# Kernel optimization log

Measured on AMD Instinct MI355X. Metric: run time of the kernel, lower is better.

Reference implementation:

```python
import jax, jax.numpy as jnp
import numpy as np

# Model dims (match init_kwargs)
B, L, C = 4, 4096, 1024   # batch, seq_len, dim
M = 128                   # memory_dim
P = 4                     # n_persistent
S = 64                    # segment_size
H = 8                     # num_heads in nn.MultiheadAttention


def _ln(x, g, b, eps=1e-5):
    mu = jnp.mean(x, -1, keepdims=True)
    var = jnp.mean((x - mu) ** 2, -1, keepdims=True)
    return (x - mu) * jax.lax.rsqrt(var + eps) * g + b


def setup_inputs() -> dict:
    key = jax.random.key(0)
    ks = jax.random.split(key, 16)
    def n(k, shape, s=0.02):
        return jax.random.normal(k, shape, jnp.float32) * s
    return {
        "x": jax.random.normal(ks[0], (B, L, C), jnp.float32),
        "persistent_memory": n(ks[1], (1, P, C)),
        "Wq": n(ks[2], (C, C)),            # query_proj (no bias)
        "Wk": n(ks[3], (C, C)),            # key_proj (no bias)
        "Wv": n(ks[4], (C, C)),            # value_proj (no bias)
        # NeuralMemoryModule.memory_net: Linear(C->M), SiLU, LN(M), Linear(M->M), LN(M)
        "mem_W1": n(ks[5], (M, C)), "mem_b1": jnp.zeros((M,)),
        "mem_ln1_g": jnp.ones((M,)), "mem_ln1_b": jnp.zeros((M,)),
        "mem_W2": n(ks[6], (M, M)), "mem_b2": jnp.zeros((M,)),
        "mem_ln2_g": jnp.ones((M,)), "mem_ln2_b": jnp.zeros((M,)),
        "mem_out_W": n(ks[7], (C, M)), "mem_out_b": jnp.zeros((C,)),
        "memory_state": jnp.zeros((1, M)),  # persistent buffer (zeros at init)
        # nn.MultiheadAttention in/out projections
        "mha_Wq": n(ks[8], (C, C)), "mha_bq": jnp.zeros((C,)),
        "mha_Wk": n(ks[9], (C, C)), "mha_bk": jnp.zeros((C,)),
        "mha_Wv": n(ks[10], (C, C)), "mha_bv": jnp.zeros((C,)),
        "mha_Wo": n(ks[11], (C, C)), "mha_bo": jnp.zeros((C,)),
        "gn_g": jnp.ones((C,)), "gn_b": jnp.zeros((C,)),   # gate_norm
        "gate_W": n(ks[12], (C, C)), "gate_b": jnp.zeros((C,)),
        "out_W": n(ks[13], (C, C)), "out_b": jnp.zeros((C,)),
    }


def reference(x, persistent_memory, Wq, Wk, Wv,
              mem_W1, mem_b1, mem_ln1_g, mem_ln1_b,
              mem_W2, mem_b2, mem_ln2_g, mem_ln2_b,
              mem_out_W, mem_out_b, memory_state,
              mha_Wq, mha_bq, mha_Wk, mha_bk, mha_Wv, mha_bv, mha_Wo, mha_bo,
              gn_g, gn_b, gate_W, gate_b, out_W, out_b):
    Bx, Lx, Cx = x.shape
    n_seg = Lx // S
    # Eval-mode: memory_state is frozen, so all segments are independent ->
    # process every segment in parallel instead of a Python loop over L.
    xs = x.reshape(Bx * n_seg, S, Cx)           # [N, S, C]
    q_seg = xs @ Wq.T                            # query_proj
    # retrieve from long-term memory: memory_net(queries) + memory_state -> output_proj
    h = jax.nn.silu(q_seg @ mem_W1.T + mem_b1)
    h = _ln(h, mem_ln1_g, mem_ln1_b)
    h = h @ mem_W2.T + mem_b2
    h = _ln(h, mem_ln2_g, mem_ln2_b)             # [N, S, M]
    retrieved = (h + memory_state[0]) @ mem_out_W.T + mem_out_b  # [N, S, C]
    # context = [retrieved_memory, persistent_memory, current_segment]
    pm = jnp.broadcast_to(persistent_memory, (Bx * n_seg, P, Cx))
    context = jnp.concatenate([retrieved, pm, xs], axis=1)       # [N, T, C], T=S+P+S
    k_in = context @ Wk.T
    v_in = context @ Wv.T
    T = context.shape[1]
    hd = Cx // H
    q = (q_seg @ mha_Wq.T + mha_bq).reshape(-1, S, H, hd)
    k = (k_in @ mha_Wk.T + mha_bk).reshape(-1, T, H, hd)
    v = (v_in @ mha_Wv.T + mha_bv).reshape(-1, T, H, hd)
    scores = jnp.einsum('nshd,nthd->nhst', q, k) / jnp.sqrt(jnp.float32(hd))
    attn = jnp.einsum('nhst,nthd->nshd', jax.nn.softmax(scores, -1), v)
    attn = attn.reshape(-1, S, Cx) @ mha_Wo.T + mha_bo           # [N, S, C]
    # learned gate blend + output projection
    gate = jax.nn.sigmoid(_ln(attn, gn_g, gn_b) @ gate_W.T + gate_b)
    out = (gate * attn + xs) @ out_W.T + out_b
    return out.reshape(Bx, Lx, Cx)
```

## Files before the change

### kernel.cpp

```cpp
#include <hip/hip_runtime.h>
#include <hip/hip_bf16.h>
#include <math.h>


using bf16 = __hip_bfloat16;

typedef __attribute__((ext_vector_type(8))) short bf16x8;
typedef __attribute__((ext_vector_type(4))) float f32x4;

__device__ __forceinline__ float ldf(const bf16* p) { return __bfloat162float(*p); }
__device__ __forceinline__ float ldf(const float* p) { return *p; }
__device__ __forceinline__ void stf(bf16* p, float v) { *p = __float2bfloat16(v); }
__device__ __forceinline__ void stf(float* p, float v) { *p = v; }
__device__ __forceinline__ float b2f(const bf16& b) { return __bfloat162float(b); }
__device__ __forceinline__ float bsf(short s) {
  union { unsigned u; float f; } cv;
  cv.u = (unsigned)(unsigned short)s << 16;
  return cv.f;
}

enum { ACT_NONE = 0, ACT_SILU = 1, ACT_SIGMOID = 2, ACT_GATE = 3, ACT_PSILU = 4 };

__global__ void detect_kernel(const unsigned short* g, int* flag) {
  if (threadIdx.x == 0) *flag = (g[0] != 0) ? 1 : 0;
}

struct ConvArgs {
  const void* src[29];
  bf16* dst[29];
  int n[29];
  int bstart[30];
};

__global__ __launch_bounds__(256) void convall_kernel(ConvArgs a, const int* __restrict__ flag) {
  int b = blockIdx.x;
  int ti = 0;
  while (ti < 28 && b >= a.bstart[ti + 1]) ++ti;
  int i = (b - a.bstart[ti]) * 256 + threadIdx.x;
  if (i >= a.n[ti]) return;
  if (*flag) a.dst[ti][i] = ((const bf16*)a.src[ti])[i];
  else a.dst[ti][i] = __float2bfloat16(((const float*)a.src[ti])[i]);
}

__global__ __launch_bounds__(256) void conv_kernel(
    const void* __restrict__ src, bf16* __restrict__ dst, int n, size_t src_off,
    const int* __restrict__ flag) {
  int i = blockIdx.x * 256 + threadIdx.x;
  if (i >= n) return;
  if (*flag) dst[i] = ((const bf16*)src)[src_off + i];
  else dst[i] = __float2bfloat16(((const float*)src)[src_off + i]);
}

__global__ __launch_bounds__(256) void pack_bias4(
    const bf16* __restrict__ bk, const bf16* __restrict__ bv,
    const bf16* __restrict__ bq, const bf16* __restrict__ b1,
    bf16* __restrict__ o) {
  int j = blockIdx.x * 256 + threadIdx.x;
  if (j >= 3200) return;
  float v;
  if (j < 1024) v = b2f(bk[j]);
  else if (j < 2048) v = b2f(bv[j - 1024]);
  else if (j < 3072) v = b2f(bq[j - 2048]);
  else v = b2f(b1[j - 3072]);
  o[j] = __float2bfloat16(v);
}

__global__ __launch_bounds__(256) void transpose_kernel(
    const bf16* __restrict__ srcb, bf16* __restrict__ dstb, int rows, int cols) {
  __shared__ unsigned short t[64][72];
  const unsigned short* src = (const unsigned short*)srcb;
  unsigned short* dst = (unsigned short*)dstb;
  const int r0 = blockIdx.y * 64, c0 = blockIdx.x * 64;
  for (int e = threadIdx.x; e < 64 * 8; e += 256) {
    int r = e >> 3, c8 = e & 7;
    uint4 v = *(const uint4*)(src + (size_t)(r0 + r) * cols + c0 + c8 * 8);
    *(uint4*)&t[r][c8 * 8] = v;
  }
  __syncthreads();
  for (int e = threadIdx.x; e < 64 * 8; e += 256) {
    int c = e >> 3, r8 = (e & 7) * 8;
    unsigned short v[8];
#pragma unroll
    for (int j = 0; j < 8; ++j) v[j] = t[r8 + j][c];
    *(uint4*)(dst + (size_t)(c0 + c) * rows + r0 + r8) = *(uint4*)v;
  }
}

__global__ __launch_bounds__(256) void kpvp_kernel(
    const bf16* __restrict__ pmb, const bf16* __restrict__ mobb,
    const bf16* __restrict__ Wb, const bf16* __restrict__ bias4b,
    bf16* __restrict__ kp, bf16* __restrict__ vp, bf16* __restrict__ bkv)
{
  const short* pm = (const short*)pmb;
  const short* mob = (const short*)mobb;
  const short* W = (const short*)Wb;
  const int wave = threadIdx.x >> 6, lane = threadIdx.x & 63;
  const int c = blockIdx.x * 4 + wave;
  const short* wrow = W + (size_t)c * 1024 + lane * 16;
  const bf16x8 w0 = *(const bf16x8*)wrow;
  const bf16x8 w1 = *(const bf16x8*)(wrow + 8);
  float acc[5];
#pragma unroll
  for (int m = 0; m < 5; ++m) {
    const short* prow = (m < 4) ? (pm + m * 1024 + lane * 16) : (mob + lane * 16);
    const bf16x8 p0 = *(const bf16x8*)prow;
    const bf16x8 p1 = *(const bf16x8*)(prow + 8);
    float s = 0.f;
#pragma unroll
    for (int j = 0; j < 8; ++j) s += bsf(w0[j]) * bsf(p0[j]) + bsf(w1[j]) * bsf(p1[j]);
    acc[m] = s;
  }
#pragma unroll
  for (int d = 1; d < 64; d <<= 1) {
#pragma unroll
    for (int m = 0; m < 5; ++m) acc[m] += __shfl_xor(acc[m], d);
  }
  if (lane == 0) {
    const float bv = b2f(bias4b[c]);
    bf16* dst = (c < 1024) ? (kp + c) : (vp + (c - 1024));
#pragma unroll
    for (int m = 0; m < 4; ++m) stf(dst + m * 1024, acc[m] + bv);
    stf(&bkv[c], acc[4] + bv);
  }
}

__device__ __forceinline__ void gl_lds16(const short* g, short* l) {
  __builtin_amdgcn_global_load_lds(
      (const __attribute__((address_space(1))) void*)g,
      (__attribute__((address_space(3))) void*)l, 16, 0, 0);
}

template <typename TC, int ACT, bool HAS_BIAS>
__global__ __launch_bounds__(256) void mgemm(
    const bf16* __restrict__ Ab, const bf16* __restrict__ Bw,
    const bf16* __restrict__ bias, TC* __restrict__ C,
    int M, int N, int K, int lda, int ldc,
    const bf16* __restrict__ ao, const void* __restrict__ xsrc, size_t xoff,
    const int* __restrict__ flag, int pn)
{
  __shared__ short As[128 * 32];
  __shared__ short Bs[128 * 32];
  const short* A = (const short*)Ab;
  const short* B = (const short*)Bw;
  const int tid = threadIdx.x;
  const int m0 = blockIdx.y * 128, n0 = blockIdx.x * 128;
  const int wave = tid >> 6, lane = tid & 63;
  const int wm = (wave & 1) * 64, wn = (wave >> 1) * 64;
  const int fm = lane & 15;
  const int fk = (lane >> 4) * 8;

  const int srow = tid >> 2, scol = (tid & 3) * 8;
  const short* gA0 = A + (size_t)(m0 + srow) * lda + scol;
  const short* gA1 = A + (size_t)(m0 + 64 + srow) * lda + scol;
  const short* gB0 = B + (size_t)(n0 + srow) * K + scol;
  const short* gB1 = B + (size_t)(n0 + 64 + srow) * K + scol;
  short* lA0 = As + tid * 8;
  short* lA1 = As + (256 + tid) * 8;
  short* lB0 = Bs + tid * 8;
  short* lB1 = Bs + (256 + tid) * 8;

  f32x4 acc[4][4] = {};

  for (int k0 = 0; k0 < K; k0 += 32) {
    gl_lds16(gA0 + k0, lA0);
    gl_lds16(gA1 + k0, lA1);
    gl_lds16(gB0 + k0, lB0);
    gl_lds16(gB1 + k0, lB1);
    __syncthreads();
    bf16x8 af[4], bfr[4];
#pragma unroll
    for (int i = 0; i < 4; ++i)
      af[i] = *(const bf16x8*)&As[(wm + i * 16 + fm) * 32 + fk];
#pragma unroll
    for (int j = 0; j < 4; ++j)
      bfr[j] = *(const bf16x8*)&Bs[(wn + j * 16 + fm) * 32 + fk];
#pragma unroll
    for (int i = 0; i < 4; ++i)
#pragma unroll
      for (int j = 0; j < 4; ++j)
        acc[i][j] = __builtin_amdgcn_mfma_f32_16x16x32_bf16(af[i], bfr[j], acc[i][j], 0, 0, 0);
    __syncthreads();
  }

  const int rg = (lane >> 4) * 4;
#pragma unroll
  for (int i = 0; i < 4; ++i) {
#pragma unroll
    for (int j = 0; j < 4; ++j) {
      const int n = n0 + wn + j * 16 + fm;
      float bv = 0.f;
      if (HAS_BIAS) bv = b2f(bias[n]);
#pragma unroll
      for (int r = 0; r < 4; ++r) {
        const int m = m0 + wm + i * 16 + rg + r;
        float v = acc[i][j][r] + bv;
        if (ACT == ACT_SILU) v = v / (1.f + __expf(-v));
        if (ACT == ACT_PSILU) { if (n >= pn) v = v / (1.f + __expf(-v)); }
        if (ACT == ACT_SIGMOID) v = 1.f / (1.f + __expf(-v));
        if (ACT == ACT_GATE) {
          v = 1.f / (1.f + __expf(-v));
          const size_t e = (size_t)m * 1024 + n;
          const float xv = *flag ? b2f(((const bf16*)xsrc)[xoff + e])
                                 : ((const float*)xsrc)[xoff + e];
          v = v * b2f(ao[e]) + xv;
        }
        stf(&C[(size_t)m * ldc + n], v);
      }
    }
  }
}

template <typename TI, typename TO, bool ADD, int W, int BS>
__global__ __launch_bounds__(BS) void ln_kernel(
    const TI* __restrict__ in, const bf16* __restrict__ g, const bf16* __restrict__ b,
    const bf16* __restrict__ addv, TO* __restrict__ out, int ldin)
{
  __shared__ float red[BS];
  const int row = blockIdx.x;
  const TI* rin = in + (size_t)row * ldin;
  TO* rout = out + (size_t)row * W;
  const int NP = W / BS;
  float v[NP];
  float s = 0.f;
#pragma unroll
  for (int i = 0; i < NP; ++i) { v[i] = ldf(&rin[threadIdx.x + i * BS]); s += v[i]; }
  red[threadIdx.x] = s; __syncthreads();
  for (int o = BS / 2; o > 0; o >>= 1) {
    if (threadIdx.x < o) red[threadIdx.x] += red[threadIdx.x + o];
    __syncthreads();
  }
  const float mean = red[0] / W;
  __syncthreads();
  float sq = 0.f;
#pragma unroll
  for (int i = 0; i < NP; ++i) { float d = v[i] - mean; sq += d * d; }
  red[threadIdx.x] = sq; __syncthreads();
  for (int o = BS / 2; o > 0; o >>= 1) {
    if (threadIdx.x < o) red[threadIdx.x] += red[threadIdx.x + o];
    __syncthreads();
  }
  const float rstd = rsqrtf(red[0] / W + 1e-5f);
#pragma unroll
  for (int i = 0; i < NP; ++i) {
    int c = threadIdx.x + i * BS;
    float o_ = (v[i] - mean) * rstd * b2f(g[c]) + b2f(b[c]);
    if (ADD) o_ += b2f(addv[c]);
    stf(&rout[c], o_);
  }
}

__global__ __launch_bounds__(512) void attn_kernel(
    const bf16* __restrict__ qg, int str_q,
    const bf16* __restrict__ krv, int str_r,
    const bf16* __restrict__ kxv, int str_x, const bf16* __restrict__ kpg,
    const bf16* __restrict__ vpg, bf16* __restrict__ outg)
{
  __shared__ short qs[4 * 64 * 32];
  __shared__ short ksl[4 * 144 * 32];
  __shared__ short vt[128 * 168];
  __shared__ short pl[64 * 168];

  const int tid = threadIdx.x;
  const int seg = blockIdx.x >> 3, h = blockIdx.x & 7;
  const unsigned short* q = (const unsigned short*)qg + (size_t)seg * 64 * str_q + h * 128;
  const unsigned short* kv_r = (const unsigned short*)krv + (size_t)seg * 64 * str_r + h * 128;
  const unsigned short* kv_x = (const unsigned short*)kxv + (size_t)seg * 64 * str_x + h * 128;
  const unsigned short* kp = (const unsigned short*)kpg;
  const unsigned short* vp = (const unsigned short*)vpg;
  const size_t obase = (size_t)seg * 64 * 1024 + h * 128;

  for (int ch = tid; ch < 64 * 16; ch += 512) {
    int row = ch >> 4, k8 = ch & 15;
    uint4 v = *(const uint4*)(q + (size_t)row * str_q + k8 * 8);
    *(uint4*)&qs[((k8 >> 2) * 64 + row) * 32 + (k8 & 3) * 8] = v;
  }
  for (int ch = tid; ch < 132 * 16; ch += 512) {
    int t = ch >> 4, k8 = ch & 15;
    const unsigned short* src;
    if (t < 64) src = kv_r + (size_t)t * str_r;
    else if (t < 68) src = kp + (size_t)(t - 64) * 1024 + h * 128;
    else src = kv_x + (size_t)(t - 68) * str_x;
    uint4 v = *(const uint4*)(src + k8 * 8);
    *(uint4*)&ksl[((k8 >> 2) * 144 + t) * 32 + (k8 & 3) * 8] = v;
  }
  __syncthreads();

  const int wave = tid >> 6, lane = tid & 63;
  const int fm = lane & 15, fq = lane >> 4;

  if (wave < 4) {
    const int s0 = wave * 16;
    f32x4 acc[10];
#pragma unroll
    for (int tt = 0; tt < 10; ++tt) acc[tt] = (f32x4){0.f, 0.f, 0.f, 0.f};
#pragma unroll
    for (int kb = 0; kb < 4; ++kb) {
      const bf16x8 a = *(const bf16x8*)&qs[(kb * 64 + s0 + fm) * 32 + fq * 8];
#pragma unroll
      for (int tt = 0; tt < 9; ++tt) {
        const bf16x8 b = *(const bf16x8*)&ksl[(kb * 144 + tt * 16 + fm) * 32 + fq * 8];
        acc[tt] = __builtin_amdgcn_mfma_f32_16x16x32_bf16(a, b, acc[tt], 0, 0, 0);
      }
    }
    const float scale = 0.08838834764831845f;
#pragma unroll
    for (int r = 0; r < 4; ++r) {
      float m = -3.0e38f;
#pragma unroll
      for (int tt = 0; tt < 9; ++tt) {
        int t = tt * 16 + fm;
        if (t < 132) m = fmaxf(m, acc[tt][r] * scale);
      }
      for (int d = 1; d < 16; d <<= 1) m = fmaxf(m, __shfl_xor(m, d));
      float e[10];
      float sum = 0.f;
#pragma unroll
      for (int tt = 0; tt < 10; ++tt) {
        int t = tt * 16 + fm;
        float ev = 0.f;
        if (t < 132) ev = __expf(acc[tt][r] * scale - m);
        e[tt] = ev; sum += ev;
      }
      for (int d = 1; d < 16; d <<= 1) sum += __shfl_xor(sum, d);
      const float inv = 1.f / sum;
      const int s = s0 + fq * 4 + r;
#pragma unroll
      for (int tt = 0; tt < 10; ++tt) {
        bf16 pv = __float2bfloat16(e[tt] * inv);
        pl[s * 168 + tt * 16 + fm] = *(const short*)&pv;
      }
    }
  } else {
    for (int ch = tid - 256; ch < 132 * 32; ch += 256) {
      int t = ch >> 5, d4 = (ch & 31) * 4;
      const unsigned short* src;
      if (t < 64) src = kv_r + 1024 + (size_t)t * str_r;
      else if (t < 68) src = vp + (size_t)(t - 64) * 1024 + h * 128;
      else src = kv_x + 1024 + (size_t)(t - 68) * str_x;
      uint2 w = *(const uint2*)(src + d4);
      vt[(d4 + 0) * 168 + t] = (short)(w.x & 0xffffu);
      vt[(d4 + 1) * 168 + t] = (short)(w.x >> 16);
      vt[(d4 + 2) * 168 + t] = (short)(w.y & 0xffffu);
      vt[(d4 + 3) * 168 + t] = (short)(w.y >> 16);
    }
    for (int ch = tid - 256; ch < 128 * 32; ch += 256) {
      int d = ch >> 5, tp = 132 + (ch & 31);
      vt[d * 168 + tp] = 0;
    }
  }
  __syncthreads();

  const int dt = wave;
  bf16x8 af[5];
#pragma unroll
  for (int kb = 0; kb < 5; ++kb)
    af[kb] = *(const bf16x8*)&vt[(dt * 16 + fm) * 168 + kb * 32 + fq * 8];
#pragma unroll
  for (int st = 0; st < 4; ++st) {
    f32x4 o = (f32x4){0.f, 0.f, 0.f, 0.f};
#pragma unroll
    for (int kb = 0; kb < 5; ++kb) {
      const bf16x8 bp = *(const bf16x8*)&pl[(st * 16 + fm) * 168 + kb * 32 + fq * 8];
      o = __builtin_amdgcn_mfma_f32_16x16x32_bf16(af[kb], bp, o, 0, 0, 0);
    }
    const int s = st * 16 + fm;
    bf16 b0 = __float2bfloat16(o[0]), b1 = __float2bfloat16(o[1]);
    bf16 b2 = __float2bfloat16(o[2]), b3 = __float2bfloat16(o[3]);
    uint2 w;
    w.x = ((unsigned)(*(unsigned short*)&b1) << 16) | (*(unsigned short*)&b0);
    w.y = ((unsigned)(*(unsigned short*)&b3) << 16) | (*(unsigned short*)&b2);
    *(uint2*)((unsigned short*)outg + obase + (size_t)s * 1024 + dt * 16 + fq * 4) = w;
  }
}

extern "C" void kernel_launch(void* const* d_in, const int* in_sizes, int n_in,
                              void* d_out, int out_size, void* d_ws, size_t ws_size,
                              hipStream_t stream)
{
  (void)n_in; (void)out_size;
  const int R = 16384, Cd = 1024;

  char* ws = (char*)d_ws;
  size_t off = 0;
  auto alloc = [&](size_t bytes) -> void* {
    void* p = ws + off;
    off += (bytes + 255) & ~(size_t)255;
    return p;
  };

  int* flag = (int*)alloc(256);
  bf16* W4    = (bf16*)alloc((size_t)3200 * Cd * sizeof(bf16));
  bf16* bias4 = (bf16*)alloc(3200 * sizeof(bf16));
  bf16* T     = (bf16*)alloc((size_t)Cd * Cd * sizeof(bf16));
  bf16* Wc    = (bf16*)alloc((size_t)2048 * 128 * sizeof(bf16));
  bf16* kp    = (bf16*)alloc((size_t)4 * Cd * sizeof(bf16));
  bf16* vp    = (bf16*)alloc((size_t)4 * Cd * sizeof(bf16));
  bf16* bkv   = (bf16*)alloc(2048 * sizeof(bf16));
  bf16* nb[30];
  nb[0] = nullptr;
  for (int i = 1; i < 30; ++i) nb[i] = (bf16*)alloc((size_t)in_sizes[i] * sizeof(bf16));
  const size_t fixed_end = off;

  size_t avail = (ws_size > fixed_end + (1u << 20)) ? (ws_size - fixed_end - (1u << 20)) : 0;
  int crmax = (int)(avail / 17152);
  if (crmax > R) crmax = R;
  if (crmax < 128) crmax = 128;
  int nch = (R + crmax - 1) / crmax;
  int CR = ((R / nch + 127) / 128) * 128;
  while (CR * nch < R) CR += 128;

  const size_t RB = (size_t)CR * Cd * sizeof(bf16);
  bf16* Xc  = (bf16*)alloc(RB);
  bf16* QS4 = (bf16*)alloc((size_t)CR * 3200 * sizeof(bf16));
  bf16* h1b = (bf16*)alloc((size_t)CR * 128 * sizeof(bf16));
  bf16* h2b = (bf16*)alloc((size_t)CR * 128 * sizeof(bf16));
  bf16* Bb  = (bf16*)alloc(RB);
  bf16* KVr = (bf16*)alloc(2 * RB);
  bf16* Cc  = (bf16*)alloc(RB);

  dim3 blk(256);
  auto g128 = [](int M_, int N_) { return dim3((unsigned)(N_ / 128), (unsigned)(M_ / 128)); };

  detect_kernel<<<1, 64, 0, stream>>>((const unsigned short*)d_in[24], flag);
  {
    ConvArgs a;
    int bs = 0;
    for (int i = 1; i < 30; ++i) {
      a.src[i - 1] = d_in[i];
      a.dst[i - 1] = nb[i];
      a.n[i - 1] = in_sizes[i];
      a.bstart[i - 1] = bs;
      bs += (in_sizes[i] + 255) / 256;
    }
    a.bstart[29] = bs;
    convall_kernel<<<dim3((unsigned)bs), blk, 0, stream>>>(a, flag);
  }
  const bf16 *pm = nb[1], *Wq = nb[2], *Wk = nb[3], *Wv = nb[4];
  const bf16 *mem_W1 = nb[5], *mem_b1 = nb[6], *ln1g = nb[7], *ln1b = nb[8];
  const bf16 *mem_W2 = nb[9], *mem_b2 = nb[10], *ln2g = nb[11], *ln2b = nb[12];
  const bf16 *mem_oW = nb[13], *mem_ob = nb[14], *mstate = nb[15];
  const bf16 *mhaWq = nb[16], *mhabq = nb[17], *mhaWk = nb[18], *mhabk = nb[19];
  const bf16 *mhaWv = nb[20], *mhabv = nb[21], *mhaWo = nb[22], *mhabo = nb[23];
  const bf16 *gn_g = nb[24], *gn_b = nb[25], *gateW = nb[26], *gateb = nb[27];
  const bf16 *outW = nb[28], *outb = nb[29];
  bf16* Wkk = W4;
  bf16* Wvv = W4 + (size_t)1024 * Cd;
  bf16* Wqq = W4 + (size_t)2048 * Cd;
  bf16* Wm1 = W4 + (size_t)3072 * Cd;

  transpose_kernel<<<dim3(16, 16), blk, 0, stream>>>(Wk, T, 1024, 1024);
  mgemm<bf16, ACT_NONE, false><<<g128(1024, 1024), blk, 0, stream>>>(
      mhaWk, T, nullptr, Wkk, 1024, 1024, 1024, 1024, 1024, nullptr, nullptr, 0, nullptr, 0);
  transpose_kernel<<<dim3(16, 16), blk, 0, stream>>>(Wv, T, 1024, 1024);
  mgemm<bf16, ACT_NONE, false><<<g128(1024, 1024), blk, 0, stream>>>(
      mhaWv, T, nullptr, Wvv, 1024, 1024, 1024, 1024, 1024, nullptr, nullptr, 0, nullptr, 0);
  transpose_kernel<<<dim3(16, 16), blk, 0, stream>>>(Wq, T, 1024, 1024);
  mgemm<bf16, ACT_NONE, false><<<g128(1024, 1024), blk, 0, stream>>>(
      mhaWq, T, nullptr, Wqq, 1024, 1024, 1024, 1024, 1024, nullptr, nullptr, 0, nullptr, 0);
  mgemm<bf16, ACT_NONE, false><<<g128(128, 1024), blk, 0, stream>>>(
      mem_W1, T, nullptr, Wm1, 128, 1024, 1024, 1024, 1024, nullptr, nullptr, 0, nullptr, 0);
  transpose_kernel<<<dim3(2, 16), blk, 0, stream>>>(mem_oW, T, 1024, 128);
  mgemm<bf16, ACT_NONE, false><<<g128(2048, 128), blk, 0, stream>>>(
      W4, T, nullptr, Wc, 2048, 128, 1024, 1024, 128, nullptr, nullptr, 0, nullptr, 0);
  pack_bias4<<<13, blk, 0, stream>>>(mhabk, mhabv, mhabq, mem_b1, bias4);
  kpvp_kernel<<<dim3(512), blk, 0, stream>>>(pm, mem_ob, W4, bias4, kp, vp, bkv);

  for (int r0 = 0; r0 < R; r0 += CR) {
    const int cr = (R - r0 < CR) ? (R - r0) : CR;
    const int n = cr * Cd;
    conv_kernel<<<dim3((n + 255) / 256), blk, 0, stream>>>(d_in[0], Xc, n, (size_t)r0 * Cd, flag);

    mgemm<bf16, ACT_PSILU, true><<<g128(cr, 3200), blk, 0, stream>>>(
        Xc, W4, bias4, QS4, cr, 3200, 1024, 1024, 3200, nullptr, nullptr, 0, nullptr, 3072);

    ln_kernel<bf16, bf16, false, 128, 128><<<cr, 128, 0, stream>>>(
        QS4 + 3072, ln1g, ln1b, nullptr, h2b, 3200);
    mgemm<bf16, ACT_NONE, true><<<g128(cr, 128), blk, 0, stream>>>(
        h2b, mem_W2, mem_b2, h1b, cr, 128, 128, 128, 128, nullptr, nullptr, 0, nullptr, 0);
    ln_kernel<bf16, bf16, true, 128, 128><<<cr, 128, 0, stream>>>(h1b, ln2g, ln2b, mstate, h2b, 128);
    mgemm<bf16, ACT_NONE, true><<<g128(cr, 2048), blk, 0, stream>>>(
        h2b, Wc, bkv, KVr, cr, 2048, 128, 128, 2048, nullptr, nullptr, 0, nullptr, 0);

    attn_kernel<<<dim3((cr / 64) * 8), dim3(512), 0, stream>>>(
        QS4 + 2048, 3200, KVr, 2048, QS4, 3200, kp, vp, Xc);

    mgemm<bf16, ACT_NONE, true><<<g128(cr, Cd), blk, 0, stream>>>(
        Xc, mhaWo, mhabo, Bb, cr, Cd, Cd, Cd, Cd, nullptr, nullptr, 0, nullptr, 0);
    ln_kernel<bf16, bf16, false, 1024, 256><<<cr, 256, 0, stream>>>(Bb, gn_g, gn_b, nullptr, Cc, Cd);
    mgemm<bf16, ACT_GATE, true><<<g128(cr, Cd), blk, 0, stream>>>(
        Cc, gateW, gateb, Xc, cr, Cd, Cd, Cd, Cd, Bb, d_in[0], (size_t)r0 * Cd, flag, 0);
    mgemm<float, ACT_NONE, true><<<g128(cr, Cd), blk, 0, stream>>>(
        Xc, outW, outb, (float*)d_out + (size_t)r0 * Cd, cr, Cd, Cd, Cd, Cd,
        nullptr, nullptr, 0, nullptr, 0);
  }
}
```

Measured before the change: 952.7 us.

## Split-K weight-folding GEMMs, stack Wq/W1, swap grid axes, XCD-remap attention

Adds a split-K GEMM (4-way K split into fp32 partials plus a reduction kernel) for the weight pre-multiplication GEMMs, which launch few blocks. Mem W1 and MHA Wq are stacked into one buffer so a single GEMM covers both. It also swaps the grid x/y mapping in the main GEMM so consecutive blocks walk M, and remaps attention block IDs so neighbouring segments land on the same XCD. The goal is more parallelism in the small setup GEMMs and better cache locality, at the cost of extra fp32 partial traffic and extra launches.

```diff
diff --git a/kernel.cpp b/kernel.cpp
--- a/kernel.cpp
+++ b/kernel.cpp
@@ -143,7 +143,7 @@
   const short* A = (const short*)Ab;
   const short* B = (const short*)Bw;
   const int tid = threadIdx.x;
-  const int m0 = blockIdx.y * 128, n0 = blockIdx.x * 128;
+  const int m0 = blockIdx.x * 128, n0 = blockIdx.y * 128;
   const int wave = tid >> 6, lane = tid & 63;
   const int wm = (wave & 1) * 64, wn = (wave >> 1) * 64;
   const int fm = lane & 15;
@@ -210,6 +210,78 @@
   }
 }
 
+__global__ __launch_bounds__(256) void kgemm(
+    const bf16* __restrict__ Ab, const bf16* __restrict__ Bw,
+    float* __restrict__ P, int M, int N, int K, int lda)
+{
+  __shared__ short As[128 * 32];
+  __shared__ short Bs[128 * 32];
+  const short* A = (const short*)Ab;
+  const short* B = (const short*)Bw;
+  const int tid = threadIdx.x;
+  const int m0 = blockIdx.x * 128, n0 = blockIdx.y * 128;
+  const int kb = blockIdx.z * (K >> 2), ke = kb + (K >> 2);
+  const int wave = tid >> 6, lane = tid & 63;
+  const int wm = (wave & 1) * 64, wn = (wave >> 1) * 64;
+  const int fm = lane & 15;
+  const int fk = (lane >> 4) * 8;
+
+  const int srow = tid >> 2, scol = (tid & 3) * 8;
+  const short* gA0 = A + (size_t)(m0 + srow) * lda + scol;
+  const short* gA1 = A + (size_t)(m0 + 64 + srow) * lda + scol;
+  const short* gB0 = B + (size_t)(n0 + srow) * K + scol;
+  const short* gB1 = B + (size_t)(n0 + 64 + srow) * K + scol;
+  short* lA0 = As + tid * 8;
+  short* lA1 = As + (256 + tid) * 8;
+  short* lB0 = Bs + tid * 8;
+  short* lB1 = Bs + (256 + tid) * 8;
+
+  f32x4 acc[4][4] = {};
+
+  for (int k0 = kb; k0 < ke; k0 += 32) {
+    gl_lds16(gA0 + k0, lA0);
+    gl_lds16(gA1 + k0, lA1);
+    gl_lds16(gB0 + k0, lB0);
+    gl_lds16(gB1 + k0, lB1);
+    __syncthreads();
+    bf16x8 af[4], bfr[4];
+#pragma unroll
+    for (int i = 0; i < 4; ++i)
+      af[i] = *(const bf16x8*)&As[(wm + i * 16 + fm) * 32 + fk];
+#pragma unroll
+    for (int j = 0; j < 4; ++j)
+      bfr[j] = *(const bf16x8*)&Bs[(wn + j * 16 + fm) * 32 + fk];
+#pragma unroll
+    for (int i = 0; i < 4; ++i)
+#pragma unroll
+      for (int j = 0; j < 4; ++j)
+        acc[i][j] = __builtin_amdgcn_mfma_f32_16x16x32_bf16(af[i], bfr[j], acc[i][j], 0, 0, 0);
+    __syncthreads();
+  }
+
+  float* Cp = P + (size_t)blockIdx.z * ((size_t)M * N);
+  const int rg = (lane >> 4) * 4;
+#pragma unroll
+  for (int i = 0; i < 4; ++i)
+#pragma unroll
+    for (int j = 0; j < 4; ++j) {
+      const int n = n0 + wn + j * 16 + fm;
+#pragma unroll
+      for (int r = 0; r < 4; ++r) {
+        const int m = m0 + wm + i * 16 + rg + r;
+        Cp[(size_t)m * N + n] = acc[i][j][r];
+      }
+    }
+}
+
+__global__ __launch_bounds__(256) void foldfin_kernel(
+    const float* __restrict__ P, bf16* __restrict__ o, int MN) {
+  int i = blockIdx.x * 256 + threadIdx.x;
+  if (i >= MN) return;
+  float s = P[i] + P[i + (size_t)MN] + P[i + 2 * (size_t)MN] + P[i + 3 * (size_t)MN];
+  o[i] = __float2bfloat16(s);
+}
+
 template <typename TI, typename TO, bool ADD, int W, int BS>
 __global__ __launch_bounds__(BS) void ln_kernel(
     const TI* __restrict__ in, const bf16* __restrict__ g, const bf16* __restrict__ b,
@@ -261,7 +333,14 @@
   __shared__ short pl[64 * 168];
 
   const int tid = threadIdx.x;
-  const int seg = blockIdx.x >> 3, h = blockIdx.x & 7;
+  unsigned bid = blockIdx.x;
+  {
+    const unsigned nwg = gridDim.x;
+    const unsigned q_ = nwg >> 3, r_ = nwg & 7;
+    const unsigned xcd = bid & 7, loc = bid >> 3;
+    bid = (xcd < r_ ? xcd * (q_ + 1) : r_ * (q_ + 1) + (xcd - r_) * q_) + loc;
+  }
+  const int seg = (int)(bid >> 3), h = (int)(bid & 7);
   const unsigned short* q = (const unsigned short*)qg + (size_t)seg * 64 * str_q + h * 128;
   const unsigned short* kv_r = (const unsigned short*)krv + (size_t)seg * 64 * str_r + h * 128;
   const unsigned short* kv_x = (const unsigned short*)kxv + (size_t)seg * 64 * str_x + h * 128;
@@ -396,9 +475,12 @@
   bf16* kp    = (bf16*)alloc((size_t)4 * Cd * sizeof(bf16));
   bf16* vp    = (bf16*)alloc((size_t)4 * Cd * sizeof(bf16));
   bf16* bkv   = (bf16*)alloc(2048 * sizeof(bf16));
+  bf16* WqStk = (bf16*)alloc((size_t)1152 * Cd * sizeof(bf16));
   bf16* nb[30];
   nb[0] = nullptr;
   for (int i = 1; i < 30; ++i) nb[i] = (bf16*)alloc((size_t)in_sizes[i] * sizeof(bf16));
+  nb[16] = WqStk;
+  nb[5]  = WqStk + (size_t)1024 * Cd;
   const size_t fixed_end = off;
 
   size_t avail = (ws_size > fixed_end + (1u << 20)) ? (ws_size - fixed_end - (1u << 20)) : 0;
@@ -409,6 +491,7 @@
   int CR = ((R / nch + 127) / 128) * 128;
   while (CR * nch < R) CR += 128;
 
+  const size_t chunk_start = off;
   const size_t RB = (size_t)CR * Cd * sizeof(bf16);
   bf16* Xc  = (bf16*)alloc(RB);
   bf16* QS4 = (bf16*)alloc((size_t)CR * 3200 * sizeof(bf16));
@@ -417,9 +500,10 @@
   bf16* Bb  = (bf16*)alloc(RB);
   bf16* KVr = (bf16*)alloc(2 * RB);
   bf16* Cc  = (bf16*)alloc(RB);
+  const size_t chunk_bytes = off - chunk_start;
 
   dim3 blk(256);
-  auto g128 = [](int M_, int N_) { return dim3((unsigned)(N_ / 128), (unsigned)(M_ / 128)); };
+  auto g128 = [](int M_, int N_) { return dim3((unsigned)(M_ / 128), (unsigned)(N_ / 128)); };
 
   detect_kernel<<<1, 64, 0, stream>>>((const unsigned short*)d_in[24], flag);
   {
@@ -448,20 +532,37 @@
   bf16* Wqq = W4 + (size_t)2048 * Cd;
   bf16* Wm1 = W4 + (size_t)3072 * Cd;
 
-  transpose_kernel<<<dim3(16, 16), blk, 0, stream>>>(Wk, T, 1024, 1024);
-  mgemm<bf16, ACT_NONE, false><<<g128(1024, 1024), blk, 0, stream>>>(
-      mhaWk, T, nullptr, Wkk, 1024, 1024, 1024, 1024, 1024, nullptr, nullptr, 0, nullptr, 0);
-  transpose_kernel<<<dim3(16, 16), blk, 0, stream>>>(Wv, T, 1024, 1024);
-  mgemm<bf16, ACT_NONE, false><<<g128(1024, 1024), blk, 0, stream>>>(
-      mhaWv, T, nullptr, Wvv, 1024, 1024, 1024, 1024, 1024, nullptr, nullptr, 0, nullptr, 0);
-  transpose_kernel<<<dim3(16, 16), blk, 0, stream>>>(Wq, T, 1024, 1024);
-  mgemm<bf16, ACT_NONE, false><<<g128(1024, 1024), blk, 0, stream>>>(
-      mhaWq, T, nullptr, Wqq, 1024, 1024, 1024, 1024, 1024, nullptr, nullptr, 0, nullptr, 0);
-  mgemm<bf16, ACT_NONE, false><<<g128(128, 1024), blk, 0, stream>>>(
-      mem_W1, T, nullptr, Wm1, 128, 1024, 1024, 1024, 1024, nullptr, nullptr, 0, nullptr, 0);
-  transpose_kernel<<<dim3(2, 16), blk, 0, stream>>>(mem_oW, T, 1024, 128);
-  mgemm<bf16, ACT_NONE, false><<<g128(2048, 128), blk, 0, stream>>>(
-      W4, T, nullptr, Wc, 2048, 128, 1024, 1024, 128, nullptr, nullptr, 0, nullptr, 0);
+  const bool use_ks = chunk_bytes >= (size_t)4 * 1152 * 1024 * sizeof(float);
+  if (use_ks) {
+    float* P = (float*)Xc;
+    transpose_kernel<<<dim3(16, 16), blk, 0, stream>>>(Wq, T, 1024, 1024);
+    kgemm<<<dim3(9, 8, 4), blk, 0, stream>>>(WqStk, T, P, 1152, 1024, 1024, 1024);
+    foldfin_kernel<<<dim3(4608), blk, 0, stream>>>(P, Wqq, 1152 * 1024);
+    transpose_kernel<<<dim3(16, 16), blk, 0, stream>>>(Wk, T, 1024, 1024);
+    kgemm<<<dim3(8, 8, 4), blk, 0, stream>>>(mhaWk, T, P, 1024, 1024, 1024, 1024);
+    foldfin_kernel<<<dim3(4096), blk, 0, stream>>>(P, Wkk, 1024 * 1024);
+    transpose_kernel<<<dim3(16, 16), blk, 0, stream>>>(Wv, T, 1024, 1024);
+    kgemm<<<dim3(8, 8, 4), blk, 0, stream>>>(mhaWv, T, P, 1024, 1024, 1024, 1024);
+    foldfin_kernel<<<dim3(4096), blk, 0, stream>>>(P, Wvv, 1024 * 1024);
+    transpose_kernel<<<dim3(2, 16), blk, 0, stream>>>(mem_oW, T, 1024, 128);
+    kgemm<<<dim3(16, 1, 4), blk, 0, stream>>>(W4, T, P, 2048, 128, 1024, 1024);
+    foldfin_kernel<<<dim3(1024), blk, 0, stream>>>(P, Wc, 2048 * 128);
+  } else {
+    transpose_kernel<<<dim3(16, 16), blk, 0, stream>>>(Wq, T, 1024, 1024);
+    mgemm<bf16, ACT_NONE, false><<<g128(1024, 1024), blk, 0, stream>>>(
+        mhaWq, T, nullptr, Wqq, 1024, 1024, 1024, 1024, 1024, nullptr, nullptr, 0, nullptr, 0);
+    mgemm<bf16, ACT_NONE, false><<<g128(128, 1024), blk, 0, stream>>>(
+        mem_W1, T, nullptr, Wm1, 128, 1024, 1024, 1024, 1024, nullptr, nullptr, 0, nullptr, 0);
+    transpose_kernel<<<dim3(16, 16), blk, 0, stream>>>(Wk, T, 1024, 1024);
+    mgemm<bf16, ACT_NONE, false><<<g128(1024, 1024), blk, 0, stream>>>(
+        mhaWk, T, nullptr, Wkk, 1024, 1024, 1024, 1024, 1024, nullptr, nullptr, 0, nullptr, 0);
+    transpose_kernel<<<dim3(16, 16), blk, 0, stream>>>(Wv, T, 1024, 1024);
+    mgemm<bf16, ACT_NONE, false><<<g128(1024, 1024), blk, 0, stream>>>(
+        mhaWv, T, nullptr, Wvv, 1024, 1024, 1024, 1024, 1024, nullptr, nullptr, 0, nullptr, 0);
+    transpose_kernel<<<dim3(2, 16), blk, 0, stream>>>(mem_oW, T, 1024, 128);
+    mgemm<bf16, ACT_NONE, false><<<g128(2048, 128), blk, 0, stream>>>(
+        W4, T, nullptr, Wc, 2048, 128, 1024, 1024, 128, nullptr, nullptr, 0, nullptr, 0);
+  }
   pack_bias4<<<13, blk, 0, stream>>>(mhabk, mhabv, mhabq, mem_b1, bias4);
   kpvp_kernel<<<dim3(512), blk, 0, stream>>>(pm, mem_ob, W4, bias4, kp, vp, bkv);
 
```

Measured after the change: 884.1 us. 1.08x faster.
